# Kernel optimization log

Hardware: AMD Instinct MI355X
Metric: run time of the kernel (lower is better)

Reference implementation:

```python
import jax, jax.numpy as jnp
import numpy as np
from jax import lax

DT = 1.0 / 120.0
B, T = 4096, 128
TWO_PI = 2.0 * np.pi


def setup_inputs() -> dict:
    key = jax.random.key(0)
    k1, k2, k3, k4 = jax.random.split(key, 4)
    return {
        "params": jax.random.normal(k1, (4,), jnp.float32),
        "covariance_params": jax.random.normal(k2, (7,), jnp.float32),
        "init_states": jax.random.normal(k3, (B, 6), jnp.float32),
        "measurements": jax.random.normal(k4, (B, T, 3), jnp.float32),
    }


def _wrap(a):
    # wrap angle innovation to [-pi, pi]
    return a - TWO_PI * jnp.round(a / TWO_PI)


def _smooth_loss(params, covariance_params, init_state, z):
    # z: [T, 3] measurements of (x, y, theta)
    friction = (jnp.tanh(params[0]) + 1.0) * 0.01
    damping = (jnp.tanh(params[1]) + 1.0) * 0.01
    cp = jax.nn.sigmoid(covariance_params)
    R = jnp.diag(cp[:3])                                    # [3,3] meas noise
    Q = jnp.diag(cp[jnp.array([3, 3, 4, 4, 5, 6])])         # [6,6] proc noise
    I6 = jnp.eye(6, dtype=z.dtype)
    Hm = jnp.zeros((3, 6), z.dtype).at[0, 0].set(1.).at[1, 1].set(1.).at[2, 4].set(1.)
    P0 = 0.01 * I6

    def f_and_F(s):
        # free-sliding puck dynamics: [x, y, dx, dy, th, dth]
        x, y, dx, dy, th, dth = s
        ndx = dx - DT * (damping * dx + friction * jnp.tanh(100. * dx))
        ndy = dy - DT * (damping * dy + friction * jnp.tanh(100. * dy))
        ndth = dth * (1.0 - DT * damping)
        ns = jnp.stack([x + DT * dx, y + DT * dy, ndx, ndy, th + DT * dth, ndth])
        gx = 1.0 - DT * (damping + friction * 100. * (1. - jnp.tanh(100. * dx) ** 2))
        gy = 1.0 - DT * (damping + friction * 100. * (1. - jnp.tanh(100. * dy) ** 2))
        F = (I6.at[0, 2].set(DT).at[1, 3].set(DT).at[4, 5].set(DT)
               .at[2, 2].set(gx).at[3, 3].set(gy).at[5, 5].set(1.0 - DT * damping))
        return ns, F

    def ekf_step(carry, zt):
        s, P = carry
        sp, F = f_and_F(s)
        Pp = F @ P @ F.T + Q
        S = Hm @ Pp @ Hm.T + R
        innov = zt - Hm @ sp
        innov = innov.at[2].set(_wrap(innov[2]))
        K = jnp.linalg.solve(S, Hm @ Pp).T          # Pp H^T S^-1
        s_new = sp + K @ innov
        P_new = (I6 - K @ Hm) @ Pp
        return (s_new, P_new), (s_new, P_new, sp, Pp, F)

    _, (sf, Pf, sp, Pp, Fs) = lax.scan(ekf_step, (init_state, P0), z)

    # RTS backward pass
    def rts_step(carry, inp):
        s_next, P_next = carry
        s_f, P_f, sp_n, Pp_n, F_n = inp
        G = jnp.linalg.solve(Pp_n, F_n @ P_f).T     # P_f F^T Pp^{-1}
        s_s = s_f + G @ (s_next - sp_n)
        P_s = P_f + G @ (P_next - Pp_n) @ G.T
        return (s_s, P_s), (s_s, P_s)

    inp = (sf[:-1], Pf[:-1], sp[1:], Pp[1:], Fs[1:])
    _, (s_sm_head, P_sm_head) = lax.scan(rts_step, (sf[-1], Pf[-1]), inp, reverse=True)
    s_sm = jnp.concatenate([s_sm_head, sf[-1:]], 0)   # [T,6]
    P_sm = jnp.concatenate([P_sm_head, Pf[-1:]], 0)   # [T,6,6]

    # log-lik style loss vs measurements[2:] (as in compute_loss)
    zz, st, Pt = z[2:], s_sm[2:], P_sm[2:]
    Sv = jnp.einsum('ij,tjk,lk->til', Hm, Pt, Hm) + R  # [T-2,3,3] meas-space var
    innov_xy = zz[:, :2] - st[:, :2]
    a = zz[:, 2] - st[:, 4]
    a = jnp.where(a > 1.5 * np.pi, a - TWO_PI, a)
    a = jnp.where(a < -1.5 * np.pi, a + TWO_PI, a)
    innov = jnp.concatenate([innov_xy, a[:, None]], 1)
    sign, logdet = jnp.linalg.slogdet(Sv)
    return jnp.sum(sign * jnp.exp(logdet) + jnp.einsum('ti,tij,tj->t', innov, Sv, innov))


def reference(params, covariance_params, init_states, measurements):
    per_seg = jax.vmap(_smooth_loss, in_axes=(None, None, 0, 0))(
        params, covariance_params, init_states, measurements)
    return jnp.sum(per_seg)
```

## Files before the change

### kernel.cpp

```cpp
#include <hip/hip_runtime.h>
#include <cmath>


namespace {

constexpr int B = 4096;
constexpr int T = 128;
constexpr int NT = B * 3;
constexpr int CPB = 64;
constexpr int NBLK = NT / CPB;
constexpr int RBLK = 256;
constexpr int RTH = 256;

constexpr float DTc     = 1.0f / 120.0f;
constexpr float TWO_PIc = 6.28318530717958647692f;
constexpr float PI_1_5  = 4.71238898038468985769f;
constexpr float INV_2PI = 0.15915494309189533577f;

__device__ __forceinline__ float frcp(float x) { return __builtin_amdgcn_rcpf(x); }

__device__ __forceinline__ float fast_tanh(float x) {
  float e = __expf(2.0f * x);
  return 1.0f - 2.0f * frcp(e + 1.0f);
}
__device__ __forceinline__ float sigmoidf(float x) {
  return frcp(1.0f + __expf(-x));
}

__global__ __launch_bounds__(256) void ztrans_kernel(
    const float* __restrict__ z, float* __restrict__ zt) {
  __shared__ float tile[96 * 65];
  const int tid = threadIdx.x;
  const int bs = blockIdx.x & 63;
  const int bt = blockIdx.x >> 6;
  const int s0 = bs * 64, t0 = bt * 32;

  const float* __restrict__ zbase = z + (size_t)s0 * 384 + t0 * 3;
#pragma unroll
  for (int k = 0; k < 6; k++) {
    const int idx = tid + k * 256;
    const int sl = idx / 24;
    const int c4 = idx - sl * 24;
    const float4 v4 = *(const float4*)(zbase + (size_t)sl * 384 + c4 * 4);
    tile[(c4 * 4 + 0) * 65 + sl] = v4.x;
    tile[(c4 * 4 + 1) * 65 + sl] = v4.y;
    tile[(c4 * 4 + 2) * 65 + sl] = v4.z;
    tile[(c4 * 4 + 3) * 65 + sl] = v4.w;
  }
  __syncthreads();
#pragma unroll
  for (int k = 0; k < 24; k++) {
    const int idx = tid + k * 256;
    const int r  = idx >> 6;
    const int sl = idx & 63;
    const int fc = r >> 5;
    const int tl = r & 31;
    zt[((size_t)fc * T + t0 + tl) * B + s0 + sl] = tile[(tl * 3 + fc) * 65 + sl];
  }
}

__global__ __launch_bounds__(CPB, 1) void filt_kernel(
    const float* __restrict__ params, const float* __restrict__ covp,
    const float* __restrict__ init_states, const float* __restrict__ zt,
    float2* __restrict__ aq) {
  const int lane = threadIdx.x;
  const int blk  = blockIdx.x;
  const int f    = blk >> 6;
  const int seq  = ((blk & 63) << 6) + lane;

  __shared__ float4 h4s[127 * CPB];
  __shared__ float  p11s[T * CPB];

  const float friction = (fast_tanh(params[0]) + 1.0f) * 0.01f;
  const float damping  = (fast_tanh(params[1]) + 1.0f) * 0.01f;
  float cp[7];
#pragma unroll
  for (int i = 0; i < 7; i++) cp[i] = sigmoidf(covp[i]);
  const float dcoef = 1.0f - DTc * damping;
  const bool isTH = (f == 2);
  const float q0 = isTH ? cp[5] : cp[3];
  const float q1 = isTH ? cp[6] : cp[4];
  const float r  = cp[f];

  const int pidx = (f == 0) ? 0 : (f == 1) ? 1 : 4;
  const int vidx = (f == 0) ? 2 : (f == 1) ? 3 : 5;
  float p = init_states[seq * 6 + pidx];
  float v = init_states[seq * 6 + vidx];
  float P00 = 0.01f, P01 = 0.0f, P11 = 0.01f;

  const float* __restrict__ ztf = zt + (size_t)f * T * B + seq;

  float zr[8];
#pragma unroll
  for (int k = 0; k < 8; k++) zr[k] = ztf[(size_t)k * B];

#pragma unroll 8
  for (int t = 0; t < T; t++) {
    const float zc = zr[t & 7];
    const int tf = (t < T - 8) ? t + 8 : T - 1;
    zr[t & 7] = ztf[(size_t)tf * B];

    float g, tv;
    if (!isTH) {
      const float th = fast_tanh(100.0f * v);
      tv = v - DTc * (damping * v + friction * th);
      g = 1.0f - DTc * (damping + 100.0f * friction * (1.0f - th * th));
    } else {
      tv = dcoef * v;
      g = dcoef;
    }
    const float tp = p + DTc * v;
    const float u = P01 + DTc * P11;
    const float Pp00 = P00 + DTc * P01 + DTc * u + q0;
    const float Pp01 = g * u;
    const float Pp11 = g * (g * P11) + q1;
    const float iS = frcp(Pp00 + r);
    const float K0 = Pp00 * iS;
    const float K1 = Pp01 * iS;
    float e = zc - tp;
    if (isTH) e = e - TWO_PIc * rintf(e * INV_2PI);
    p = tp + K0 * e;
    v = tv + K1 * e;
    const float om = 1.0f - K0;
    P00 = om * Pp00;
    P01 = om * Pp01;
    P11 = Pp11 - K1 * Pp01;

    if (t < 127) h4s[t * CPB + lane] = make_float4(p, v, P00, P01);
    p11s[t * CPB + lane] = P11;
  }

  {
    float e = ztf[(size_t)(T - 1) * B] - p;
    if (isTH) {
      if (e >  PI_1_5) e -= TWO_PIc;
      if (e < -PI_1_5) e += TWO_PIc;
    }
    const float a = P00 + r;
    aq[((size_t)f * T + (T - 1)) * B + seq] = make_float2(a, a * e * e);
  }

  float sp_ = p, sv_ = v, Ps00 = P00, Ps01 = P01, Ps11 = P11;

  float4 h4r[2];
  float  p11r[2];
  float  zrb[8];
  h4r[0]  = h4s[126 * CPB + lane];
  p11r[0] = p11s[126 * CPB + lane];
  h4r[1]  = h4s[125 * CPB + lane];
  p11r[1] = p11s[125 * CPB + lane];
#pragma unroll
  for (int k = 0; k < 8; k++) zrb[k] = ztf[(size_t)(126 - k) * B];

#pragma unroll 8
  for (int i = 0; i < 128; i++) {
    const int n = 126 - i;
    const int s2 = i & 1;
    const int s8 = i & 7;
    const float4 h4 = h4r[s2];
    const float f11 = p11r[s2];
    const float zn_ = zrb[s8];
    const int nl = (n >= 4) ? n - 2 : 2;
    h4r[s2]  = h4s[nl * CPB + lane];
    p11r[s2] = p11s[nl * CPB + lane];
    const int nz = (n >= 10) ? n - 8 : 2;
    zrb[s8] = ztf[(size_t)nz * B];

    const float fp = h4.x, fv = h4.y, f00 = h4.z, f01 = h4.w;

    float g, tv;
    if (!isTH) {
      const float th = fast_tanh(100.0f * fv);
      tv = fv - DTc * (damping * fv + friction * th);
      g = 1.0f - DTc * (damping + 100.0f * friction * (1.0f - th * th));
    } else {
      tv = dcoef * fv;
      g = dcoef;
    }
    const float tp = fp + DTc * fv;
    const float u = f01 + DTc * f11;
    const float Pp00 = f00 + DTc * f01 + DTc * u + q0;
    const float Pp01 = g * u;
    const float Pp11 = g * (g * f11) + q1;

    const float idet = frcp(Pp00 * Pp11 - Pp01 * Pp01);
    const float W00 = f00, W01 = DTc * f00 + g * f01;
    const float W10 = f01, W11 = DTc * f01 + g * f11;
    const float G00 = (W00 * Pp11 - W01 * Pp01) * idet;
    const float G01 = (W01 * Pp00 - W00 * Pp01) * idet;
    const float G10 = (W10 * Pp11 - W11 * Pp01) * idet;
    const float G11 = (W11 * Pp00 - W10 * Pp01) * idet;

    const float ds0 = sp_ - tp, ds1 = sv_ - tv;
    const float np = fp + G00 * ds0 + G01 * ds1;
    const float nv = fv + G10 * ds0 + G11 * ds1;

    const float M00 = Ps00 - Pp00, M01 = Ps01 - Pp01, M11 = Ps11 - Pp11;
    const float GM00 = G00 * M00 + G01 * M01, GM01 = G00 * M01 + G01 * M11;
    const float GM10 = G10 * M00 + G11 * M01, GM11 = G10 * M01 + G11 * M11;
    Ps00 = f00 + GM00 * G00 + GM01 * G01;
    Ps01 = f01 + GM00 * G10 + GM01 * G11;
    Ps11 = f11 + GM10 * G10 + GM11 * G11;
    sp_ = np;
    sv_ = nv;

    if (n >= 2) {
      const float a = Ps00 + r;
      float e = zn_ - np;
      if (isTH) {
        if (e >  PI_1_5) e -= TWO_PIc;
        if (e < -PI_1_5) e += TWO_PIc;
      }
      aq[((size_t)f * T + n) * B + seq] = make_float2(a, a * e * e);
    }
  }
}

__global__ __launch_bounds__(RTH) void reduce_kernel(
    const float2* __restrict__ aq, float* __restrict__ out) {
  const int tid = threadIdx.x;
  constexpr int NTERM = 126 * B;
  float part = 0.0f;
  for (int idx = blockIdx.x * RTH + tid; idx < NTERM; idx += RTH * RBLK) {
    const int t = 2 + (idx >> 12);
    const int s = idx & (B - 1);
    const float2 a0 = aq[((size_t)0 * T + t) * B + s];
    const float2 a1 = aq[((size_t)1 * T + t) * B + s];
    const float2 a2 = aq[((size_t)2 * T + t) * B + s];
    part += a0.x * a1.x * a2.x + (a0.y + a1.y + a2.y);
  }
#pragma unroll
  for (int off = 32; off > 0; off >>= 1) part += __shfl_down(part, off);
  __shared__ float red[RTH / 64];
  if ((tid & 63) == 0) red[tid >> 6] = part;
  __syncthreads();
  if (tid == 0) {
    float s = 0.0f;
#pragma unroll
    for (int w = 0; w < RTH / 64; w++) s += red[w];
    atomicAdd(out, s);
  }
}

}

extern "C" void kernel_launch(void* const* d_in, const int* in_sizes, int n_in,
                              void* d_out, int out_size, void* d_ws, size_t ws_size,
                              hipStream_t stream) {
  const float* params      = (const float*)d_in[0];
  const float* covp        = (const float*)d_in[1];
  const float* init_states = (const float*)d_in[2];
  const float* z           = (const float*)d_in[3];
  float* out = (float*)d_out;

  const size_t ztB = (size_t)T * NT * sizeof(float);
  const size_t aqB = (size_t)T * NT * sizeof(float2);
  const size_t needBytes = ztB + aqB;

  hipMemsetAsync(d_out, 0, sizeof(float), stream);

  if (ws_size >= needBytes) {
    float*  ztp = (float*)d_ws;
    float2* aqp = (float2*)((char*)d_ws + ztB);
    ztrans_kernel<<<256, 256, 0, stream>>>(z, ztp);
    filt_kernel<<<NBLK, CPB, 0, stream>>>(params, covp, init_states, ztp, aqp);
    reduce_kernel<<<RBLK, RTH, 0, stream>>>(aqp, out);
  }
}
```

Baseline: 124.2 us.

## Software-pipeline RTS smoother gain computation and vectorize reduction loads

The backward smoother loop now computes the state-independent quantities (predicted state, predicted covariance, smoother gain) for step i+2 ahead of time, since they depend only on stored filter results. Only the short dependent chain through the smoothed state and covariance stays on the critical path. The LDS prefetch depth grows from 2 to 4 to feed this. The reduce kernel now reads float4 (two elements per load) and uses more blocks. The cost is higher register pressure from the extra prefetch buffers and the two in-flight Der structs.

New measurement: 129.0 us. 3.9% more time.

```diff
diff --git a/kernel.cpp b/kernel.cpp
--- a/kernel.cpp
+++ b/kernel.cpp
@@ -9,7 +9,7 @@
 constexpr int NT = B * 3;
 constexpr int CPB = 64;
 constexpr int NBLK = NT / CPB;
-constexpr int RBLK = 256;
+constexpr int RBLK = 512;
 constexpr int RTH = 256;
 
 constexpr float DTc     = 1.0f / 120.0f;
@@ -25,6 +25,42 @@
 }
 __device__ __forceinline__ float sigmoidf(float x) {
   return frcp(1.0f + __expf(-x));
+}
+
+struct Der {
+  float tp, tv, Pp00, Pp01, Pp11;
+  float G00, G01, G10, G11;
+};
+
+__device__ __forceinline__ Der derive(const float4 h4, const float f11,
+                                      const float damping, const float friction,
+                                      const float dcoef, const float q0,
+                                      const float q1, const bool isTH) {
+  Der d;
+  const float fp = h4.x, fv = h4.y, f00 = h4.z, f01 = h4.w;
+  float g;
+  if (!isTH) {
+    const float th = fast_tanh(100.0f * fv);
+    d.tv = fv - DTc * (damping * fv + friction * th);
+    g = 1.0f - DTc * (damping + 100.0f * friction * (1.0f - th * th));
+  } else {
+    d.tv = dcoef * fv;
+    g = dcoef;
+  }
+  d.tp = fp + DTc * fv;
+  const float u = f01 + DTc * f11;
+  d.Pp00 = f00 + DTc * f01 + DTc * u + q0;
+  d.Pp01 = g * u;
+  d.Pp11 = g * (g * f11) + q1;
+  const float idet = frcp(d.Pp00 * d.Pp11 - d.Pp01 * d.Pp01);
+  const float c0 = d.Pp11 * idet, c1 = d.Pp01 * idet, c2 = d.Pp00 * idet;
+  const float W01 = DTc * f00 + g * f01;
+  const float W11 = DTc * f01 + g * f11;
+  d.G00 = f00 * c0 - W01 * c1;
+  d.G01 = W01 * c2 - f00 * c1;
+  d.G10 = f01 * c0 - W11 * c1;
+  d.G11 = W11 * c2 - f01 * c1;
+  return d;
 }
 
 __global__ __launch_bounds__(256) void ztrans_kernel(
@@ -142,65 +178,44 @@
 
   float sp_ = p, sv_ = v, Ps00 = P00, Ps01 = P01, Ps11 = P11;
 
-  float4 h4r[2];
-  float  p11r[2];
+  float4 h4r[4];
+  float  p11r[4];
   float  zrb[8];
-  h4r[0]  = h4s[126 * CPB + lane];
-  p11r[0] = p11s[126 * CPB + lane];
-  h4r[1]  = h4s[125 * CPB + lane];
-  p11r[1] = p11s[125 * CPB + lane];
+#pragma unroll
+  for (int k = 0; k < 4; k++) {
+    h4r[k]  = h4s[(126 - k) * CPB + lane];
+    p11r[k] = p11s[(126 - k) * CPB + lane];
+  }
 #pragma unroll
   for (int k = 0; k < 8; k++) zrb[k] = ztf[(size_t)(126 - k) * B];
+
+  Der dr[2];
+  dr[0] = derive(h4r[0], p11r[0], damping, friction, dcoef, q0, q1, isTH);
+  dr[1] = derive(h4r[1], p11r[1], damping, friction, dcoef, q0, q1, isTH);
 
 #pragma unroll 8
   for (int i = 0; i < 128; i++) {
     const int n = 126 - i;
+    const int s4 = i & 3;
+    const int s8 = i & 7;
     const int s2 = i & 1;
-    const int s8 = i & 7;
-    const float4 h4 = h4r[s2];
-    const float f11 = p11r[s2];
+
+    const Der d = dr[s2];
+    const float4 h4 = h4r[s4];
+    const float f11 = p11r[s4];
     const float zn_ = zrb[s8];
-    const int nl = (n >= 4) ? n - 2 : 2;
-    h4r[s2]  = h4s[nl * CPB + lane];
-    p11r[s2] = p11s[nl * CPB + lane];
-    const int nz = (n >= 10) ? n - 8 : 2;
-    zrb[s8] = ztf[(size_t)nz * B];
-
     const float fp = h4.x, fv = h4.y, f00 = h4.z, f01 = h4.w;
 
-    float g, tv;
-    if (!isTH) {
-      const float th = fast_tanh(100.0f * fv);
-      tv = fv - DTc * (damping * fv + friction * th);
-      g = 1.0f - DTc * (damping + 100.0f * friction * (1.0f - th * th));
-    } else {
-      tv = dcoef * fv;
-      g = dcoef;
-    }
-    const float tp = fp + DTc * fv;
-    const float u = f01 + DTc * f11;
-    const float Pp00 = f00 + DTc * f01 + DTc * u + q0;
-    const float Pp01 = g * u;
-    const float Pp11 = g * (g * f11) + q1;
-
-    const float idet = frcp(Pp00 * Pp11 - Pp01 * Pp01);
-    const float W00 = f00, W01 = DTc * f00 + g * f01;
-    const float W10 = f01, W11 = DTc * f01 + g * f11;
-    const float G00 = (W00 * Pp11 - W01 * Pp01) * idet;
-    const float G01 = (W01 * Pp00 - W00 * Pp01) * idet;
-    const float G10 = (W10 * Pp11 - W11 * Pp01) * idet;
-    const float G11 = (W11 * Pp00 - W10 * Pp01) * idet;
-
-    const float ds0 = sp_ - tp, ds1 = sv_ - tv;
-    const float np = fp + G00 * ds0 + G01 * ds1;
-    const float nv = fv + G10 * ds0 + G11 * ds1;
-
-    const float M00 = Ps00 - Pp00, M01 = Ps01 - Pp01, M11 = Ps11 - Pp11;
-    const float GM00 = G00 * M00 + G01 * M01, GM01 = G00 * M01 + G01 * M11;
-    const float GM10 = G10 * M00 + G11 * M01, GM11 = G10 * M01 + G11 * M11;
-    Ps00 = f00 + GM00 * G00 + GM01 * G01;
-    Ps01 = f01 + GM00 * G10 + GM01 * G11;
-    Ps11 = f11 + GM10 * G10 + GM11 * G11;
+    const float ds0 = sp_ - d.tp, ds1 = sv_ - d.tv;
+    const float np = fp + d.G00 * ds0 + d.G01 * ds1;
+    const float nv = fv + d.G10 * ds0 + d.G11 * ds1;
+
+    const float M00 = Ps00 - d.Pp00, M01 = Ps01 - d.Pp01, M11 = Ps11 - d.Pp11;
+    const float GM00 = d.G00 * M00 + d.G01 * M01, GM01 = d.G00 * M01 + d.G01 * M11;
+    const float GM10 = d.G10 * M00 + d.G11 * M01, GM11 = d.G10 * M01 + d.G11 * M11;
+    Ps00 = f00 + GM00 * d.G00 + GM01 * d.G01;
+    Ps01 = f01 + GM00 * d.G10 + GM01 * d.G11;
+    Ps11 = f11 + GM10 * d.G10 + GM11 * d.G11;
     sp_ = np;
     sv_ = nv;
 
@@ -213,21 +228,32 @@
       }
       aq[((size_t)f * T + n) * B + seq] = make_float2(a, a * e * e);
     }
+
+    dr[s2] = derive(h4r[(i + 2) & 3], p11r[(i + 2) & 3],
+                    damping, friction, dcoef, q0, q1, isTH);
+
+    const int nl = (n >= 6) ? n - 4 : 2;
+    h4r[s4]  = h4s[nl * CPB + lane];
+    p11r[s4] = p11s[nl * CPB + lane];
+    const int nz = (n >= 10) ? n - 8 : 2;
+    zrb[s8] = ztf[(size_t)nz * B];
   }
 }
 
 __global__ __launch_bounds__(RTH) void reduce_kernel(
-    const float2* __restrict__ aq, float* __restrict__ out) {
+    const float4* __restrict__ aq4, float* __restrict__ out) {
   const int tid = threadIdx.x;
-  constexpr int NTERM = 126 * B;
+  constexpr int HB = B / 2;
+  constexpr int NTERM4 = 126 * HB;
   float part = 0.0f;
-  for (int idx = blockIdx.x * RTH + tid; idx < NTERM; idx += RTH * RBLK) {
-    const int t = 2 + (idx >> 12);
-    const int s = idx & (B - 1);
-    const float2 a0 = aq[((size_t)0 * T + t) * B + s];
-    const float2 a1 = aq[((size_t)1 * T + t) * B + s];
-    const float2 a2 = aq[((size_t)2 * T + t) * B + s];
+  for (int idx = blockIdx.x * RTH + tid; idx < NTERM4; idx += RTH * RBLK) {
+    const int t = 2 + (idx >> 11);
+    const int s4 = idx & (HB - 1);
+    const float4 a0 = aq4[((size_t)0 * T + t) * HB + s4];
+    const float4 a1 = aq4[((size_t)1 * T + t) * HB + s4];
+    const float4 a2 = aq4[((size_t)2 * T + t) * HB + s4];
     part += a0.x * a1.x * a2.x + (a0.y + a1.y + a2.y);
+    part += a0.z * a1.z * a2.z + (a0.w + a1.w + a2.w);
   }
 #pragma unroll
   for (int off = 32; off > 0; off >>= 1) part += __shfl_down(part, off);
@@ -264,6 +290,6 @@
     float2* aqp = (float2*)((char*)d_ws + ztB);
     ztrans_kernel<<<256, 256, 0, stream>>>(z, ztp);
     filt_kernel<<<NBLK, CPB, 0, stream>>>(params, covp, init_states, ztp, aqp);
-    reduce_kernel<<<RBLK, RTH, 0, stream>>>(aqp, out);
-  }
-}
+    reduce_kernel<<<RBLK, RTH, 0, stream>>>((const float4*)aqp, out);
+  }
+}
```

## Fuse final reduction into filter kernel via last-block-done counters

Applied to the files above, without the earlier changes.

Removes the separate reduce kernel. Each filter block increments a per-sequence-block counter, and the third block to finish (the last of the three components) reads back all three components' aq values for its 64 sequences, sums them and atomically adds to the output. The counters are zeroed in the transpose kernel. This saves one kernel launch and its tail, at the cost of threadfence and atomic overhead and a serial 126-step reduction tail in the last blocks.

New measurement: 153.1 us. 23.4% more time.

```diff
diff --git a/kernel.cpp b/kernel.cpp
--- a/kernel.cpp
+++ b/kernel.cpp
@@ -9,8 +9,6 @@
 constexpr int NT = B * 3;
 constexpr int CPB = 64;
 constexpr int NBLK = NT / CPB;
-constexpr int RBLK = 256;
-constexpr int RTH = 256;
 
 constexpr float DTc     = 1.0f / 120.0f;
 constexpr float TWO_PIc = 6.28318530717958647692f;
@@ -28,9 +26,11 @@
 }
 
 __global__ __launch_bounds__(256) void ztrans_kernel(
-    const float* __restrict__ z, float* __restrict__ zt) {
+    const float* __restrict__ z, float* __restrict__ zt,
+    unsigned* __restrict__ cnt) {
   __shared__ float tile[96 * 65];
   const int tid = threadIdx.x;
+  if (blockIdx.x == 0 && tid < 64) cnt[tid] = 0u;
   const int bs = blockIdx.x & 63;
   const int bt = blockIdx.x >> 6;
   const int s0 = bs * 64, t0 = bt * 32;
@@ -62,11 +62,13 @@
 __global__ __launch_bounds__(CPB, 1) void filt_kernel(
     const float* __restrict__ params, const float* __restrict__ covp,
     const float* __restrict__ init_states, const float* __restrict__ zt,
-    float2* __restrict__ aq) {
+    float2* __restrict__ aq, unsigned* __restrict__ cnt,
+    float* __restrict__ out) {
   const int lane = threadIdx.x;
   const int blk  = blockIdx.x;
   const int f    = blk >> 6;
-  const int seq  = ((blk & 63) << 6) + lane;
+  const int sblk = blk & 63;
+  const int seq  = (sblk << 6) + lane;
 
   __shared__ float4 h4s[127 * CPB];
   __shared__ float  p11s[T * CPB];
@@ -214,31 +216,27 @@
       aq[((size_t)f * T + n) * B + seq] = make_float2(a, a * e * e);
     }
   }
-}
-
-__global__ __launch_bounds__(RTH) void reduce_kernel(
-    const float2* __restrict__ aq, float* __restrict__ out) {
-  const int tid = threadIdx.x;
-  constexpr int NTERM = 126 * B;
-  float part = 0.0f;
-  for (int idx = blockIdx.x * RTH + tid; idx < NTERM; idx += RTH * RBLK) {
-    const int t = 2 + (idx >> 12);
-    const int s = idx & (B - 1);
-    const float2 a0 = aq[((size_t)0 * T + t) * B + s];
-    const float2 a1 = aq[((size_t)1 * T + t) * B + s];
-    const float2 a2 = aq[((size_t)2 * T + t) * B + s];
-    part += a0.x * a1.x * a2.x + (a0.y + a1.y + a2.y);
-  }
-#pragma unroll
-  for (int off = 32; off > 0; off >>= 1) part += __shfl_down(part, off);
-  __shared__ float red[RTH / 64];
-  if ((tid & 63) == 0) red[tid >> 6] = part;
-  __syncthreads();
-  if (tid == 0) {
-    float s = 0.0f;
-#pragma unroll
-    for (int w = 0; w < RTH / 64; w++) s += red[w];
-    atomicAdd(out, s);
+
+  __threadfence();
+  unsigned old = 0;
+  if (lane == 0) old = atomicAdd(&cnt[sblk], 1u);
+  old = (unsigned)__shfl((int)old, 0);
+  if (old == 2u) {
+    __threadfence();
+    const float2* __restrict__ a0p = aq + (size_t)0 * T * B + (sblk << 6) + lane;
+    const float2* __restrict__ a1p = aq + (size_t)1 * T * B + (sblk << 6) + lane;
+    const float2* __restrict__ a2p = aq + (size_t)2 * T * B + (sblk << 6) + lane;
+    float part = 0.0f;
+#pragma unroll 4
+    for (int t = 2; t < T; t++) {
+      const float2 a0 = a0p[(size_t)t * B];
+      const float2 a1 = a1p[(size_t)t * B];
+      const float2 a2 = a2p[(size_t)t * B];
+      part += a0.x * a1.x * a2.x + (a0.y + a1.y + a2.y);
+    }
+#pragma unroll
+    for (int off = 32; off > 0; off >>= 1) part += __shfl_down(part, off);
+    if (lane == 0) atomicAdd(out, part);
   }
 }
 
@@ -253,17 +251,19 @@
   const float* z           = (const float*)d_in[3];
   float* out = (float*)d_out;
 
-  const size_t ztB = (size_t)T * NT * sizeof(float);
-  const size_t aqB = (size_t)T * NT * sizeof(float2);
-  const size_t needBytes = ztB + aqB;
+  const size_t ztB  = (size_t)T * NT * sizeof(float);
+  const size_t aqB  = (size_t)T * NT * sizeof(float2);
+  const size_t cntB = 256;
+  const size_t needBytes = ztB + aqB + cntB;
 
   hipMemsetAsync(d_out, 0, sizeof(float), stream);
 
   if (ws_size >= needBytes) {
-    float*  ztp = (float*)d_ws;
-    float2* aqp = (float2*)((char*)d_ws + ztB);
-    ztrans_kernel<<<256, 256, 0, stream>>>(z, ztp);
-    filt_kernel<<<NBLK, CPB, 0, stream>>>(params, covp, init_states, ztp, aqp);
-    reduce_kernel<<<RBLK, RTH, 0, stream>>>(aqp, out);
-  }
-}
+    float*    ztp = (float*)d_ws;
+    float2*   aqp = (float2*)((char*)d_ws + ztB);
+    unsigned* cnt = (unsigned*)((char*)d_ws + ztB + aqB);
+    ztrans_kernel<<<256, 256, 0, stream>>>(z, ztp, cnt);
+    filt_kernel<<<NBLK, CPB, 0, stream>>>(params, covp, init_states, ztp,
+                                          aqp, cnt, out);
+  }
+}
```
